# Kernel optimization log

Measured on AMD Instinct MI355X. Metric: run time of the kernel, lower is better.

The kernel has to match this reference:

```python
import jax, jax.numpy as jnp
import numpy as np

PATCH = 7
PAD = PATCH // 2  # 3


def _to_gray(x):
    # x: [B,3,H,W] -> [B,1,H,W]
    return 0.299 * x[:, 0:1] + 0.587 * x[:, 1:2] + 0.114 * x[:, 2:3]


def _census_transform(x):
    # x: [B,C,H,W] RGB -> grayscale, then 48 shifted binary comparisons.
    if x.shape[1] == 3:
        x = _to_gray(x)
    B, C, H, W = x.shape
    x_pad = jnp.pad(x, ((0, 0), (0, 0), (PAD, PAD), (PAD, PAD)), mode='reflect')
    center = x
    feats = []
    for i in range(PATCH):
        for j in range(PATCH):
            if i == PAD and j == PAD:
                continue
            neighbor = x_pad[:, :, i:i + H, j:j + W]
            feats.append((center > neighbor).astype(x.dtype))
    return jnp.concatenate(feats, axis=1)  # [B,48,H,W]


def setup_inputs() -> dict:
    key = jax.random.key(0)
    k1, k2 = jax.random.split(key)
    B, C, H, W = 8, 3, 512, 512
    pred = jax.random.uniform(k1, (B, C, H, W), dtype=jnp.float32)
    target = jax.random.uniform(k2, (B, C, H, W), dtype=jnp.float32)
    return {"pred": pred, "target": target}


def reference(pred, target):
    pred_census = _census_transform(pred)
    target_census = _census_transform(target)
    return jnp.abs(pred_census - target_census).mean()
```

## Files before the change

### kernel.cpp

```cpp
#include <hip/hip_runtime.h>


#define BATCH 8
#define HH 512
#define WW 512
#define PLANE (HH * WW)
#define TILE_W 32
#define TILE_H 64
#define LT_W 38
#define LT_H 70
#define LT_PITCH 39
#define RPT 8

__global__ __launch_bounds__(256)
void census_loss_kernel(const float* __restrict__ pred,
                        const float* __restrict__ target,
                        float* __restrict__ out) {
    __shared__ float sP[LT_H][LT_PITCH];
    __shared__ float sT[LT_H][LT_PITCH];

    const int b = blockIdx.z;
    const int ty0 = blockIdx.y * TILE_H;
    const int tx0 = blockIdx.x * TILE_W;
    const float* __restrict__ pb = pred + (size_t)b * 3 * PLANE;
    const float* __restrict__ tb = target + (size_t)b * 3 * PLANE;

    for (int idx = threadIdx.x; idx < LT_H * LT_W; idx += 256) {
        const int ly = idx / LT_W;
        const int lx = idx - ly * LT_W;
        int gy = ty0 + ly - 3;
        int gx = tx0 + lx - 3;
        gy = gy < 0 ? -gy : (gy >= HH ? 2 * HH - 2 - gy : gy);
        gx = gx < 0 ? -gx : (gx >= WW ? 2 * WW - 2 - gx : gx);
        const int off = gy * WW + gx;
        sP[ly][lx] = 0.299f * pb[off] + 0.587f * pb[off + PLANE] + 0.114f * pb[off + 2 * PLANE];
        sT[ly][lx] = 0.299f * tb[off] + 0.587f * tb[off + PLANE] + 0.114f * tb[off + 2 * PLANE];
    }
    __syncthreads();

    const int c   = threadIdx.x & 31;
    const int pr0 = (threadIdx.x >> 5) * RPT;

    float cP[RPT], cT[RPT];
    #pragma unroll
    for (int p = 0; p < RPT; ++p) {
        cP[p] = sP[pr0 + p + 3][c + 3];
        cT[p] = sT[pr0 + p + 3][c + 3];
    }

    int cnt = 0;
    #pragma unroll
    for (int j = 0; j < 7; ++j) {
        float vP[RPT + 6], vT[RPT + 6];
        #pragma unroll
        for (int i = 0; i < RPT + 6; ++i) {
            vP[i] = sP[pr0 + i][c + j];
            vT[i] = sT[pr0 + i][c + j];
        }
        #pragma unroll
        for (int p = 0; p < RPT; ++p) {
            #pragma unroll
            for (int i = 0; i < 7; ++i) {
                if (j == 3 && i == 3) continue;
                const bool bp = cP[p] > vP[p + i];
                const bool bt = cT[p] > vT[p + i];
                cnt += (bp != bt) ? 1 : 0;
            }
        }
    }

    #pragma unroll
    for (int offs = 32; offs > 0; offs >>= 1)
        cnt += __shfl_down(cnt, offs, 64);

    __shared__ int wsum[4];
    if ((threadIdx.x & 63) == 0) wsum[threadIdx.x >> 6] = cnt;
    __syncthreads();
    if (threadIdx.x == 0) {
        const int total = wsum[0] + wsum[1] + wsum[2] + wsum[3];
        atomicAdd(out, (float)total * (1.0f / 100663296.0f));
    }
}

extern "C" void kernel_launch(void* const* d_in, const int* in_sizes, int n_in,
                              void* d_out, int out_size, void* d_ws, size_t ws_size,
                              hipStream_t stream) {
    const float* pred   = (const float*)d_in[0];
    const float* target = (const float*)d_in[1];
    float* out = (float*)d_out;

    hipMemsetAsync(out, 0, sizeof(float), stream);

    dim3 grid(WW / TILE_W, HH / TILE_H, BATCH);
    census_loss_kernel<<<grid, 256, 0, stream>>>(pred, target, out);
}
```

Measured before the change: 116.7 us.

## Split grayscale into separate vectorized pass and use ballot-popcount census counting

Grayscale conversion moves into its own float4-vectorized kernel that writes gray planes to workspace, so the census kernel no longer recomputes gray values for halo pixels. The census kernel uses 32x32 tiles with a transposed shared layout and counts mismatches per wave with ballot and popcount, which drops the shuffle reduction. In exchange it adds an extra global round trip of the gray images and a second launch, and it performs many ballots per element.

After: 139.8 us. 19.8% more time.

```diff
diff --git a/kernel.cpp b/kernel.cpp
--- a/kernel.cpp
+++ b/kernel.cpp
@@ -5,36 +5,64 @@
 #define HH 512
 #define WW 512
 #define PLANE (HH * WW)
-#define TILE_W 32
-#define TILE_H 64
-#define LT_W 38
-#define LT_H 70
-#define LT_PITCH 39
-#define RPT 8
+#define PLANE4 (PLANE / 4)
+
+#define NV (BATCH * PLANE4)
 
 __global__ __launch_bounds__(256)
-void census_loss_kernel(const float* __restrict__ pred,
-                        const float* __restrict__ target,
-                        float* __restrict__ out) {
-    __shared__ float sP[LT_H][LT_PITCH];
-    __shared__ float sT[LT_H][LT_PITCH];
+void gray_kernel(const float* __restrict__ pred,
+                 const float* __restrict__ target,
+                 float* __restrict__ gp, float* __restrict__ gt) {
+    int gid = blockIdx.x * 256 + threadIdx.x;
+    const float4* src;
+    float4* dst;
+    if (gid < NV) {
+        src = (const float4*)pred;  dst = (float4*)gp;
+    } else {
+        src = (const float4*)target; dst = (float4*)gt; gid -= NV;
+    }
+    const int b  = gid >> 16;
+    const int p4 = gid & (PLANE4 - 1);
+    const int base = b * 3 * PLANE4 + p4;
+    const float4 r  = src[base];
+    const float4 g  = src[base + PLANE4];
+    const float4 bl = src[base + 2 * PLANE4];
+    float4 o;
+    o.x = 0.299f * r.x + 0.587f * g.x + 0.114f * bl.x;
+    o.y = 0.299f * r.y + 0.587f * g.y + 0.114f * bl.y;
+    o.z = 0.299f * r.z + 0.587f * g.z + 0.114f * bl.z;
+    o.w = 0.299f * r.w + 0.587f * g.w + 0.114f * bl.w;
+    dst[gid] = o;
+}
 
-    const int b = blockIdx.z;
-    const int ty0 = blockIdx.y * TILE_H;
-    const int tx0 = blockIdx.x * TILE_W;
-    const float* __restrict__ pb = pred + (size_t)b * 3 * PLANE;
-    const float* __restrict__ tb = target + (size_t)b * 3 * PLANE;
+#define TILE 32
+#define RPT 4
+#define LT 38
+#define PITCH 44
 
-    for (int idx = threadIdx.x; idx < LT_H * LT_W; idx += 256) {
-        const int ly = idx / LT_W;
-        const int lx = idx - ly * LT_W;
+__global__ __launch_bounds__(256)
+void census_kernel(const float* __restrict__ gp,
+                   const float* __restrict__ gt,
+                   float* __restrict__ out) {
+    __shared__ float sP[LT][PITCH];
+    __shared__ float sT[LT][PITCH];
+
+    const int b   = blockIdx.z;
+    const int ty0 = blockIdx.y * TILE;
+    const int tx0 = blockIdx.x * TILE;
+    const float* __restrict__ Pb = gp + (size_t)b * PLANE;
+    const float* __restrict__ Tb = gt + (size_t)b * PLANE;
+
+    for (int idx = threadIdx.x; idx < LT * LT; idx += 256) {
+        const int ly = idx / LT;
+        const int lx = idx - ly * LT;
         int gy = ty0 + ly - 3;
         int gx = tx0 + lx - 3;
         gy = gy < 0 ? -gy : (gy >= HH ? 2 * HH - 2 - gy : gy);
         gx = gx < 0 ? -gx : (gx >= WW ? 2 * WW - 2 - gx : gx);
         const int off = gy * WW + gx;
-        sP[ly][lx] = 0.299f * pb[off] + 0.587f * pb[off + PLANE] + 0.114f * pb[off + 2 * PLANE];
-        sT[ly][lx] = 0.299f * tb[off] + 0.587f * tb[off + PLANE] + 0.114f * tb[off + 2 * PLANE];
+        sP[lx][ly] = Pb[off];
+        sT[lx][ly] = Tb[off];
     }
     __syncthreads();
 
@@ -44,37 +72,32 @@
     float cP[RPT], cT[RPT];
     #pragma unroll
     for (int p = 0; p < RPT; ++p) {
-        cP[p] = sP[pr0 + p + 3][c + 3];
-        cT[p] = sT[pr0 + p + 3][c + 3];
+        cP[p] = sP[c + 3][pr0 + 3 + p];
+        cT[p] = sT[c + 3][pr0 + 3 + p];
     }
 
-    int cnt = 0;
+    long long scnt = 0;
     #pragma unroll
     for (int j = 0; j < 7; ++j) {
-        float vP[RPT + 6], vT[RPT + 6];
+        const float* __restrict__ colP = &sP[c + j][pr0];
+        const float* __restrict__ colT = &sT[c + j][pr0];
+        float wP[RPT + 6], wT[RPT + 6];
         #pragma unroll
-        for (int i = 0; i < RPT + 6; ++i) {
-            vP[i] = sP[pr0 + i][c + j];
-            vT[i] = sT[pr0 + i][c + j];
-        }
+        for (int i = 0; i < RPT + 6; ++i) { wP[i] = colP[i]; wT[i] = colT[i]; }
         #pragma unroll
         for (int p = 0; p < RPT; ++p) {
             #pragma unroll
             for (int i = 0; i < 7; ++i) {
                 if (j == 3 && i == 3) continue;
-                const bool bp = cP[p] > vP[p + i];
-                const bool bt = cT[p] > vT[p + i];
-                cnt += (bp != bt) ? 1 : 0;
+                const unsigned long long bp = __ballot(cP[p] > wP[p + i]);
+                const unsigned long long bt = __ballot(cT[p] > wT[p + i]);
+                scnt += __popcll(bp ^ bt);
             }
         }
     }
 
-    #pragma unroll
-    for (int offs = 32; offs > 0; offs >>= 1)
-        cnt += __shfl_down(cnt, offs, 64);
-
     __shared__ int wsum[4];
-    if ((threadIdx.x & 63) == 0) wsum[threadIdx.x >> 6] = cnt;
+    if ((threadIdx.x & 63) == 0) wsum[threadIdx.x >> 6] = (int)scnt;
     __syncthreads();
     if (threadIdx.x == 0) {
         const int total = wsum[0] + wsum[1] + wsum[2] + wsum[3];
@@ -88,9 +111,13 @@
     const float* pred   = (const float*)d_in[0];
     const float* target = (const float*)d_in[1];
     float* out = (float*)d_out;
+    float* gp = (float*)d_ws;
+    float* gt = gp + (size_t)BATCH * PLANE;
 
     hipMemsetAsync(out, 0, sizeof(float), stream);
 
-    dim3 grid(WW / TILE_W, HH / TILE_H, BATCH);
-    census_loss_kernel<<<grid, 256, 0, stream>>>(pred, target, out);
+    gray_kernel<<<dim3(2 * NV / 256), 256, 0, stream>>>(pred, target, gp, gt);
+
+    dim3 g2(WW / TILE, HH / TILE, BATCH);
+    census_kernel<<<g2, 256, 0, stream>>>(gp, gt, out);
 }
```

## Transpose shared-memory tile to column-major and use vectorized column window loads

Applied to the files above, without the earlier changes.

Shared tiles are now stored transposed (column-major, pitch 44) so each thread reads its vertical 10-element window with float4/float2 vector loads instead of scalar loads. The tile becomes 64 wide by 32 tall with 512 threads, each handling 4 rows of one column, and the grid is reshaped to match. The intent is fewer LDS instructions and a better load-to-halo ratio horizontally. The transposed stores during staging may cause bank conflicts, and each thread now does less work per column load.

New measurement: 101.3 us. -13.2%, faster.

```diff
diff --git a/kernel.cpp b/kernel.cpp
--- a/kernel.cpp
+++ b/kernel.cpp
@@ -5,80 +5,103 @@
 #define HH 512
 #define WW 512
 #define PLANE (HH * WW)
-#define TILE_W 32
-#define TILE_H 64
-#define LT_W 38
-#define LT_H 70
-#define LT_PITCH 39
-#define RPT 8
+#define TW 64
+#define TH 32
+#define LW 70
+#define LH 38
+#define PITCH 44
+#define NTHREADS 512
 
-__global__ __launch_bounds__(256)
-void census_loss_kernel(const float* __restrict__ pred,
-                        const float* __restrict__ target,
-                        float* __restrict__ out) {
-    __shared__ float sP[LT_H][LT_PITCH];
-    __shared__ float sT[LT_H][LT_PITCH];
+__global__ __launch_bounds__(NTHREADS, 8)
+void census_fused(const float* __restrict__ pred,
+                  const float* __restrict__ target,
+                  float* __restrict__ out) {
+    __shared__ __align__(16) float sP[LW][PITCH];
+    __shared__ __align__(16) float sT[LW][PITCH];
 
-    const int b = blockIdx.z;
-    const int ty0 = blockIdx.y * TILE_H;
-    const int tx0 = blockIdx.x * TILE_W;
+    const int b   = blockIdx.z;
+    const int ty0 = blockIdx.y * TH;
+    const int tx0 = blockIdx.x * TW;
     const float* __restrict__ pb = pred + (size_t)b * 3 * PLANE;
     const float* __restrict__ tb = target + (size_t)b * 3 * PLANE;
 
-    for (int idx = threadIdx.x; idx < LT_H * LT_W; idx += 256) {
-        const int ly = idx / LT_W;
-        const int lx = idx - ly * LT_W;
+    for (int idx = threadIdx.x; idx < LW * LH; idx += NTHREADS) {
+        const int ly = idx / LW;
+        const int lx = idx - ly * LW;
         int gy = ty0 + ly - 3;
         int gx = tx0 + lx - 3;
         gy = gy < 0 ? -gy : (gy >= HH ? 2 * HH - 2 - gy : gy);
         gx = gx < 0 ? -gx : (gx >= WW ? 2 * WW - 2 - gx : gx);
         const int off = gy * WW + gx;
-        sP[ly][lx] = 0.299f * pb[off] + 0.587f * pb[off + PLANE] + 0.114f * pb[off + 2 * PLANE];
-        sT[ly][lx] = 0.299f * tb[off] + 0.587f * tb[off + PLANE] + 0.114f * tb[off + 2 * PLANE];
+        const float p0 = pb[off], p1 = pb[off + PLANE], p2 = pb[off + 2 * PLANE];
+        const float t0 = tb[off], t1 = tb[off + PLANE], t2 = tb[off + 2 * PLANE];
+        sP[lx][ly] = 0.299f * p0 + 0.587f * p1 + 0.114f * p2;
+        sT[lx][ly] = 0.299f * t0 + 0.587f * t1 + 0.114f * t2;
     }
     __syncthreads();
 
-    const int c   = threadIdx.x & 31;
-    const int pr0 = (threadIdx.x >> 5) * RPT;
-
-    float cP[RPT], cT[RPT];
-    #pragma unroll
-    for (int p = 0; p < RPT; ++p) {
-        cP[p] = sP[pr0 + p + 3][c + 3];
-        cT[p] = sT[pr0 + p + 3][c + 3];
-    }
+    const int c   = threadIdx.x & 63;
+    const int pr0 = (threadIdx.x >> 6) * 4;
 
     int cnt = 0;
+    float cP[4], cT[4];
+
+    {
+        const float* colP = &sP[c + 3][pr0];
+        const float* colT = &sT[c + 3][pr0];
+        float wP[10], wT[10];
+        *(float4*)&wP[0] = *(const float4*)(colP);
+        *(float4*)&wP[4] = *(const float4*)(colP + 4);
+        *(float2*)&wP[8] = *(const float2*)(colP + 8);
+        *(float4*)&wT[0] = *(const float4*)(colT);
+        *(float4*)&wT[4] = *(const float4*)(colT + 4);
+        *(float2*)&wT[8] = *(const float2*)(colT + 8);
+        #pragma unroll
+        for (int p = 0; p < 4; ++p) { cP[p] = wP[3 + p]; cT[p] = wT[3 + p]; }
+        #pragma unroll
+        for (int p = 0; p < 4; ++p) {
+            #pragma unroll
+            for (int dy = -3; dy <= 3; ++dy) {
+                if (dy == 0) continue;
+                const bool bp = cP[p] > wP[3 + p + dy];
+                const bool bt = cT[p] > wT[3 + p + dy];
+                cnt += (bp != bt) ? 1 : 0;
+            }
+        }
+    }
     #pragma unroll
-    for (int j = 0; j < 7; ++j) {
-        float vP[RPT + 6], vT[RPT + 6];
+    for (int t = 0; t < 6; ++t) {
+        const int jj = (t < 3) ? t : t + 1;
+        const float* colP = &sP[c + jj][pr0];
+        const float* colT = &sT[c + jj][pr0];
+        float wP[10], wT[10];
+        *(float4*)&wP[0] = *(const float4*)(colP);
+        *(float4*)&wP[4] = *(const float4*)(colP + 4);
+        *(float2*)&wP[8] = *(const float2*)(colP + 8);
+        *(float4*)&wT[0] = *(const float4*)(colT);
+        *(float4*)&wT[4] = *(const float4*)(colT + 4);
+        *(float2*)&wT[8] = *(const float2*)(colT + 8);
         #pragma unroll
-        for (int i = 0; i < RPT + 6; ++i) {
-            vP[i] = sP[pr0 + i][c + j];
-            vT[i] = sT[pr0 + i][c + j];
-        }
-        #pragma unroll
-        for (int p = 0; p < RPT; ++p) {
+        for (int p = 0; p < 4; ++p) {
             #pragma unroll
-            for (int i = 0; i < 7; ++i) {
-                if (j == 3 && i == 3) continue;
-                const bool bp = cP[p] > vP[p + i];
-                const bool bt = cT[p] > vT[p + i];
+            for (int dy = -3; dy <= 3; ++dy) {
+                const bool bp = cP[p] > wP[3 + p + dy];
+                const bool bt = cT[p] > wT[3 + p + dy];
                 cnt += (bp != bt) ? 1 : 0;
             }
         }
     }
 
     #pragma unroll
-    for (int offs = 32; offs > 0; offs >>= 1)
-        cnt += __shfl_down(cnt, offs, 64);
-
-    __shared__ int wsum[4];
+    for (int o = 32; o > 0; o >>= 1) cnt += __shfl_down(cnt, o, 64);
+    __shared__ int wsum[8];
     if ((threadIdx.x & 63) == 0) wsum[threadIdx.x >> 6] = cnt;
     __syncthreads();
     if (threadIdx.x == 0) {
-        const int total = wsum[0] + wsum[1] + wsum[2] + wsum[3];
-        atomicAdd(out, (float)total * (1.0f / 100663296.0f));
+        int tot = 0;
+        #pragma unroll
+        for (int w = 0; w < 8; ++w) tot += wsum[w];
+        atomicAdd(out, (float)tot * (1.0f / 100663296.0f));
     }
 }
 
@@ -91,6 +114,6 @@
 
     hipMemsetAsync(out, 0, sizeof(float), stream);
 
-    dim3 grid(WW / TILE_W, HH / TILE_H, BATCH);
-    census_loss_kernel<<<grid, 256, 0, stream>>>(pred, target, out);
+    dim3 grid(WW / TW, HH / TH, BATCH);
+    census_fused<<<grid, NTHREADS, 0, stream>>>(pred, target, out);
 }
```
